# Optimization experiments

Measured on AMD Instinct MI355X. Metric: run time of the kernel, lower is better.

Reference implementation:

```python
import jax, jax.numpy as jnp
import numpy as np

H, B, D, C = 6, 512, 2048, 1000   # heads (5 ICs + backbone exit), batch, feat dim, classes
TAU = 0.5                          # confidence_threshold


def setup_inputs() -> dict:
    key = jax.random.key(0)
    k1, k2, k3, k4 = jax.random.split(key, 4)
    feats = jax.random.normal(k1, (H, B, D), dtype=jnp.float32)          # pooled reps at each exit
    W = jax.random.normal(k2, (H, D, C), dtype=jnp.float32) * 0.07       # per-head classifier weights
    b = jax.random.normal(k3, (H, C), dtype=jnp.float32) * 0.1
    y_true = jax.random.randint(k4, (B,), 0, C)
    return {"feats": feats, "W": W, "b": b, "y_true": y_true}


def reference(feats, W, b, y_true):
    # Per-head logits for every sample (vectorized replacement for the shrinking-batch loop).
    logits = jnp.einsum('hbd,hdc->hbc', feats, W) + b[:, None, :]        # [H, B, C]
    logp = jax.nn.log_softmax(logits, axis=-1)
    conf = jnp.exp(logp).max(axis=-1)                                    # [H, B] max softmax prob (prob_conf=True)

    # Early-exit routing: first head with conf >= TAU; else head with max confidence
    # (argmax returns the first occurrence, matching the strict '>' update in find_exit).
    exited = conf >= TAU                                                  # [H, B]
    any_exit = exited.any(axis=0)                                         # [B]
    first_exit = jnp.argmax(exited, axis=0)                               # [B] first True along heads
    best_conf = jnp.argmax(conf, axis=0)                                  # [B] fallback exit
    exit_idx = jnp.where(any_exit, first_exit, best_conf)                 # [B] == sample_exited_at

    # Gather the chosen head's logits per sample (vectorized masked-scatter of sample_outputs).
    outputs = jnp.take_along_axis(logits, exit_idx[None, :, None], axis=0)[0]   # [B, C]

    # criterion_ic: cross-entropy loss + accuracy on routed outputs
    out_logp = jax.nn.log_softmax(outputs, axis=-1)
    loss = -jnp.take_along_axis(out_logp, y_true[:, None], axis=1).mean()
    acc = (outputs.argmax(axis=-1) == y_true).astype(jnp.float32).mean()
    return outputs, exit_idx.astype(jnp.int32), loss, acc
```

## Files before the change

kernel.cpp:

```cpp
#include <hip/hip_runtime.h>
#include <hip/hip_bf16.h>
#include <math.h>

#define Hn 6
#define Bn 512
#define Dn 2048
#define Cn 1000
#define Cpad 1024
#define TAUv 0.5f
#define KSPLIT 2
#define KPER (Dn / KSPLIT)
#define NIT (KPER / 32)

typedef unsigned int u32;
typedef unsigned short u16;
typedef __attribute__((ext_vector_type(8))) short short8;
typedef __attribute__((ext_vector_type(4))) float f32x4;

union FragU { u32 d[4]; short8 s; };

__device__ __forceinline__ u32 cvt_pk2(float f0, float f1) {
  union { __hip_bfloat162 h; u32 u; } cv;
  cv.h = __float22bfloat162_rn(make_float2(f0, f1));
  return cv.u;
}

__device__ __forceinline__ void pack8f(const float* f, FragU& hi, FragU& lo) {
  float r[8];
#pragma unroll
  for (int i = 0; i < 4; ++i) {
    const u32 d = cvt_pk2(f[2 * i], f[2 * i + 1]);
    hi.d[i] = d;
    r[2 * i]     = f[2 * i]     - __uint_as_float(d << 16);
    r[2 * i + 1] = f[2 * i + 1] - __uint_as_float(d & 0xffff0000u);
  }
#pragma unroll
  for (int i = 0; i < 4; ++i) lo.d[i] = cvt_pk2(r[2 * i], r[2 * i + 1]);
}

__device__ __forceinline__ void dma16(const void* g, void* l) {
  __builtin_amdgcn_global_load_lds(
      (const __attribute__((address_space(1))) u32*)g,
      (__attribute__((address_space(3))) u32*)l, 16, 0, 0);
}

__global__ __launch_bounds__(256, 3) void gemm_k(
    const float* __restrict__ feats, const float* __restrict__ W,
    const float* __restrict__ bias, float* __restrict__ logits)
{
  const int h  = blockIdx.z >> 1;
  const int kz = blockIdx.z & 1;
  const int m0 = blockIdx.y * 128;
  const int n0 = blockIdx.x * 64;
  const int t = threadIdx.x, lane = t & 63, w = t >> 6;

  __shared__ __align__(16) float lds[2][6144];

  const int rA = (w & 1) * 64 + (lane >> 3);
  const int qA = (lane & 7) ^ ((lane >> 3) & 7);
  const float* gsrcA = feats + ((size_t)(h * Bn + m0 + rA)) * Dn + kz * KPER + qA * 4;
  const size_t gciA = (size_t)8 * Dn;
  const int dstA = w * 8192 + lane * 16;

  const int kb = (w - 2) * 16 + (lane >> 4);
  const int cB = lane & 15;
  const float* Wrow = W + ((size_t)h * Dn + kz * KPER) * Cn;
  const int dstB = 16384 + (w - 2) * 4096 + lane * 16;

  const int fl = lane & 15, fq = lane >> 4;
  const int wm = (w & 1) * 64, wn = (w >> 1) * 32;
  const int sxor = fl & 7;

  f32x4 acc[4][2];
#pragma unroll
  for (int i = 0; i < 4; ++i)
#pragma unroll
    for (int j = 0; j < 2; ++j) acc[i][j] = (f32x4){0.f, 0.f, 0.f, 0.f};

#define STAGE(TILE)                                                                   \
  {                                                                                   \
    char* sb = (char*)&lds[(TILE) & 1][0];                                            \
    if (w < 2) {                                                                      \
      const float* g = gsrcA + (size_t)(TILE) * 32;                                   \
      _Pragma("unroll")                                                               \
      for (int i = 0; i < 8; ++i) dma16(g + i * gciA, sb + dstA + i * 1024);          \
    } else {                                                                          \
      const size_t kt0 = (size_t)(TILE) * 32;                                         \
      _Pragma("unroll")                                                               \
      for (int i = 0; i < 4; ++i) {                                                   \
        const int kl = kb + 4 * i;                                                    \
        const int pc = cB ^ (((kl >> 3) & 1) << 2);                                   \
        int col = n0 + pc * 4;                                                        \
        col = (col + 3 < Cn) ? col : (Cn - 4);                                        \
        dma16(Wrow + (kt0 + kl) * Cn + col, sb + dstB + i * 1024);                    \
      }                                                                               \
    }                                                                                 \
  }

#define WAITCUR()                                                                     \
  {                                                                                   \
    if (w < 2) asm volatile("s_waitcnt vmcnt(8)" ::: "memory");                       \
    else       asm volatile("s_waitcnt vmcnt(4)" ::: "memory");                       \
  }

#define COMPUTE_TILE(IT)                                                              \
  {                                                                                   \
    const char*  ab = (const char*)&lds[(IT) & 1][0];                                 \
    const float* bb = (const float*)(ab + 16384);                                     \
    FragU ah[4], al[4];                                                               \
    _Pragma("unroll")                                                                 \
    for (int mt = 0; mt < 4; ++mt) {                                                  \
      const int r = wm + mt * 16 + fl;                                                \
      const float4 v0 = *(const float4*)(ab + r * 128 + ((((fq * 2)    ) ^ sxor) * 16)); \
      const float4 v1 = *(const float4*)(ab + r * 128 + ((((fq * 2) + 1) ^ sxor) * 16)); \
      float f[8] = {v0.x, v0.y, v0.z, v0.w, v1.x, v1.y, v1.z, v1.w};                  \
      pack8f(f, ah[mt], al[mt]);                                                      \
    }                                                                                 \
    _Pragma("unroll")                                                                 \
    for (int nt = 0; nt < 2; ++nt) {                                                  \
      const int n = wn + nt * 16 + fl;                                                \
      const int nsw = ((((n >> 2) ^ ((fq & 1) << 2)) << 2) | (n & 3));                \
      float f[8];                                                                     \
      _Pragma("unroll")                                                               \
      for (int e = 0; e < 8; ++e) f[e] = bb[(fq * 8 + e) * 64 + nsw];                 \
      FragU bh, bl;                                                                   \
      pack8f(f, bh, bl);                                                              \
      _Pragma("unroll")                                                               \
      for (int mt = 0; mt < 4; ++mt) {                                                \
        acc[mt][nt] = __builtin_amdgcn_mfma_f32_16x16x32_bf16(ah[mt].s, bh.s, acc[mt][nt], 0, 0, 0); \
        acc[mt][nt] = __builtin_amdgcn_mfma_f32_16x16x32_bf16(ah[mt].s, bl.s, acc[mt][nt], 0, 0, 0); \
        acc[mt][nt] = __builtin_amdgcn_mfma_f32_16x16x32_bf16(al[mt].s, bh.s, acc[mt][nt], 0, 0, 0); \
      }                                                                               \
    }                                                                                 \
  }

  STAGE(0);

  for (int it = 0; it < NIT - 1; ++it) {
    STAGE(it + 1);
    WAITCUR();
    __builtin_amdgcn_s_barrier();
    __builtin_amdgcn_sched_barrier(0);
    __builtin_amdgcn_s_setprio(1);
    COMPUTE_TILE(it);
    __builtin_amdgcn_s_setprio(0);
    __builtin_amdgcn_sched_barrier(0);
    asm volatile("s_waitcnt lgkmcnt(0)" ::: "memory");
    __builtin_amdgcn_s_barrier();
  }
  asm volatile("s_waitcnt vmcnt(0)" ::: "memory");
  __builtin_amdgcn_s_barrier();
  __builtin_amdgcn_sched_barrier(0);
  __builtin_amdgcn_s_setprio(1);
  COMPUTE_TILE(NIT - 1);
  __builtin_amdgcn_s_setprio(0);
#undef COMPUTE_TILE
#undef WAITCUR
#undef STAGE

  float* part = logits + (size_t)kz * ((size_t)Hn * Bn * Cn);
#pragma unroll
  for (int nt = 0; nt < 2; ++nt) {
    const int col = n0 + wn + nt * 16 + fl;
    if (col >= Cn) continue;
    const float bv = (kz == 0) ? bias[(size_t)h * Cn + col] : 0.f;
#pragma unroll
    for (int mt = 0; mt < 4; ++mt) {
      const int rbase = m0 + wm + mt * 16 + fq * 4;
#pragma unroll
      for (int r = 0; r < 4; ++r)
        part[((size_t)h * Bn + rbase + r) * Cn + col] = acc[mt][nt][r] + bv;
    }
  }
}

__global__ __launch_bounds__(64) void stats_k(
    const float* __restrict__ logits, float* __restrict__ msA,
    float* __restrict__ ssA, u32* __restrict__ ticket)
{
  const int id = blockIdx.x;
  const int lane = threadIdx.x;
  if (id == 0 && lane == 0) *ticket = 0;
  const size_t S = (size_t)Hn * Bn * Cn;
  const float* p = logits + (size_t)id * Cn;

  float vv[16];
#pragma unroll
  for (int i = 0; i < 4; ++i) {
    const int c4 = i * 256 + lane * 4;
    if (c4 + 3 < Cn) {
      const float4 v0 = *(const float4*)(p + c4);
      const float4 v1 = *(const float4*)(p + S + c4);
      vv[4 * i + 0] = v0.x + v1.x;
      vv[4 * i + 1] = v0.y + v1.y;
      vv[4 * i + 2] = v0.z + v1.z;
      vv[4 * i + 3] = v0.w + v1.w;
    } else {
#pragma unroll
      for (int j = 0; j < 4; ++j) {
        const int c = c4 + j;
        vv[4 * i + j] = (c < Cn) ? p[c] + p[S + c] : -3.4e38f;
      }
    }
  }
  float m = -3.4e38f;
#pragma unroll
  for (int i = 0; i < 16; ++i) m = fmaxf(m, vv[i]);
#pragma unroll
  for (int off = 32; off >= 1; off >>= 1) m = fmaxf(m, __shfl_xor(m, off));
  float s = 0.f;
#pragma unroll
  for (int i = 0; i < 16; ++i) s += (vv[i] > -3.0e38f) ? expf(vv[i] - m) : 0.f;
#pragma unroll
  for (int off = 32; off >= 1; off >>= 1) s += __shfl_xor(s, off);
  if (lane == 0) { msA[id] = m; ssA[id] = s; }
}

__global__ __launch_bounds__(256) void pick_k(
    const float* __restrict__ logits, const float* __restrict__ msA,
    const float* __restrict__ ssA, const int* __restrict__ y,
    float* __restrict__ out, float* __restrict__ out_exit,
    float* __restrict__ loss_b, float* __restrict__ corr_b,
    u32* __restrict__ ticket, float* __restrict__ scalars)
{
  const int b = blockIdx.x, tid = threadIdx.x;
  const int lane = tid & 63, w = tid >> 6;
  const size_t S = (size_t)Hn * Bn * Cn;

  int first = -1, best = 0;
  float bestc = -3.4e38f;
#pragma unroll
  for (int h = 0; h < Hn; ++h) {
    const float c = 1.0f / ssA[h * Bn + b];
    if (first < 0 && c >= TAUv) first = h;
    if (c > bestc) { bestc = c; best = h; }
  }
  const int ex = (first >= 0) ? first : best;
  const float* p = logits + ((size_t)ex * Bn + b) * Cn;

  const int c4 = tid * 4;
  float vv[4] = {-3.4e38f, -3.4e38f, -3.4e38f, -3.4e38f};
  if (c4 + 3 < Cn) {
    const float4 v0 = *(const float4*)(p + c4);
    const float4 v1 = *(const float4*)(p + S + c4);
    vv[0] = v0.x + v1.x;
    vv[1] = v0.y + v1.y;
    vv[2] = v0.z + v1.z;
    vv[3] = v0.w + v1.w;
  }
  float vm = -3.4e38f; int im = 1 << 30;
#pragma unroll
  for (int j = 0; j < 4; ++j) {
    const int c = c4 + j;
    if (c < Cn) {
      out[(size_t)b * Cn + c] = vv[j];
      if (vv[j] > vm) { vm = vv[j]; im = c; }
    }
  }
#pragma unroll
  for (int off = 32; off >= 1; off >>= 1) {
    const float ov = __shfl_xor(vm, off);
    const int   oi = __shfl_xor(im, off);
    if (ov > vm || (ov == vm && oi < im)) { vm = ov; im = oi; }
  }
  __shared__ float rm[4]; __shared__ int ri[4];
  __shared__ u32 tk;
  if (lane == 0) { rm[w] = vm; ri[w] = im; }
  __syncthreads();
  if (tid == 0) {
    float bm = rm[0]; int bi = ri[0];
    for (int q = 1; q < 4; ++q)
      if (rm[q] > bm || (rm[q] == bm && ri[q] < bi)) { bm = rm[q]; bi = ri[q]; }
    const int yt = y[b];
    const float ryt = p[yt] + p[S + yt];
    const float lp = ryt - msA[ex * Bn + b] - logf(ssA[ex * Bn + b]);
    out_exit[b] = (float)ex;
    loss_b[b] = -lp;
    corr_b[b] = (bi == yt) ? 1.f : 0.f;
    __threadfence();
    tk = atomicAdd(ticket, 1u);
  }
  __syncthreads();

  if (tk == (u32)(Bn - 1)) {
    __threadfence();
    float l = loss_b[tid] + loss_b[tid + 256];
    float c = corr_b[tid] + corr_b[tid + 256];
#pragma unroll
    for (int off = 32; off >= 1; off >>= 1) {
      l += __shfl_xor(l, off);
      c += __shfl_xor(c, off);
    }
    __shared__ float sl[4], sc[4];
    if (lane == 0) { sl[w] = l; sc[w] = c; }
    __syncthreads();
    if (tid == 0) {
      scalars[0] = (sl[0] + sl[1] + sl[2] + sl[3]) * (1.0f / (float)Bn);
      scalars[1] = (sc[0] + sc[1] + sc[2] + sc[3]) * (1.0f / (float)Bn);
    }
  }
}

extern "C" void kernel_launch(void* const* d_in, const int* in_sizes, int n_in,
                              void* d_out, int out_size, void* d_ws, size_t ws_size,
                              hipStream_t stream) {
  const float* feats = (const float*)d_in[0];
  const float* W     = (const float*)d_in[1];
  const float* bias  = (const float*)d_in[2];
  const int*   y     = (const int*)d_in[3];
  float* out = (float*)d_out;

  float* logits = (float*)d_ws;
  float* loss_b = logits + (size_t)KSPLIT * Hn * Bn * Cn;
  float* corr_b = loss_b + Bn;
  float* msA    = corr_b + Bn;
  float* ssA    = msA + Hn * Bn;
  u32*   ticket = (u32*)(ssA + Hn * Bn);
  float* out_exit    = out + (size_t)Bn * Cn;
  float* out_scalars = out + (size_t)Bn * Cn + Bn;

  gemm_k<<<dim3(Cpad / 64, Bn / 128, Hn * KSPLIT), 256, 0, stream>>>(
      feats, W, bias, logits);
  stats_k<<<Hn * Bn, 64, 0, stream>>>(logits, msA, ssA, ticket);
  pick_k<<<Bn, 256, 0, stream>>>(logits, msA, ssA, y, out, out_exit,
                                 loss_b, corr_b, ticket, out_scalars);
}
```

Before: 186.7 us.

## Fuse GEMM, softmax stats, and exit routing into one persistent kernel with grid barriers

Merges the three separate kernels into a single launch of 768 blocks that synchronize through atomic-counter grid barriers between the GEMM, row-statistics, and routing/loss stages. The stats stage maps one wave per (head, sample) row and the pick stage uses the first 512 blocks. This removes the inter-kernel launch gaps and tail drains, but adds a memset of the counters and spin-wait barriers. It relies on all blocks being co-resident, otherwise it would deadlock.

```diff
diff --git a/kernel.cpp b/kernel.cpp
--- a/kernel.cpp
+++ b/kernel.cpp
@@ -11,6 +11,7 @@
 #define KSPLIT 2
 #define KPER (Dn / KSPLIT)
 #define NIT (KPER / 32)
+#define NBLK 768
 
 typedef unsigned int u32;
 typedef unsigned short u16;
@@ -44,14 +45,31 @@
       (__attribute__((address_space(3))) u32*)l, 16, 0, 0);
 }
 
-__global__ __launch_bounds__(256, 3) void gemm_k(
+__device__ __forceinline__ void grid_barrier(u32* cnt, int tid) {
+  __syncthreads();
+  if (tid == 0) {
+    __threadfence();
+    atomicAdd(cnt, 1u);
+    while (__hip_atomic_load(cnt, __ATOMIC_RELAXED, __HIP_MEMORY_SCOPE_AGENT) < (u32)NBLK)
+      __builtin_amdgcn_s_sleep(8);
+  }
+  __syncthreads();
+  __threadfence();
+}
+
+__global__ __launch_bounds__(256, 3) void fused_k(
     const float* __restrict__ feats, const float* __restrict__ W,
-    const float* __restrict__ bias, float* __restrict__ logits)
+    const float* __restrict__ bias, float* logits,
+    const int* __restrict__ y, float* __restrict__ out,
+    float* __restrict__ out_exit, float* __restrict__ loss_b,
+    float* __restrict__ corr_b, float* __restrict__ msA,
+    float* __restrict__ ssA, u32* cnts, float* __restrict__ scalars)
 {
   const int h  = blockIdx.z >> 1;
   const int kz = blockIdx.z & 1;
   const int m0 = blockIdx.y * 128;
   const int n0 = blockIdx.x * 64;
+  const int bid = blockIdx.x + 16 * (blockIdx.y + 4 * blockIdx.z);
   const int t = threadIdx.x, lane = t & 63, w = t >> 6;
 
   __shared__ __align__(16) float lds[2][6144];
@@ -172,131 +190,120 @@
         part[((size_t)h * Bn + rbase + r) * Cn + col] = acc[mt][nt][r] + bv;
     }
   }
-}
-
-__global__ __launch_bounds__(64) void stats_k(
-    const float* __restrict__ logits, float* __restrict__ msA,
-    float* __restrict__ ssA, u32* __restrict__ ticket)
-{
-  const int id = blockIdx.x;
-  const int lane = threadIdx.x;
-  if (id == 0 && lane == 0) *ticket = 0;
+
+  grid_barrier(&cnts[0], t);
+
   const size_t S = (size_t)Hn * Bn * Cn;
-  const float* p = logits + (size_t)id * Cn;
-
-  float vv[16];
-#pragma unroll
-  for (int i = 0; i < 4; ++i) {
-    const int c4 = i * 256 + lane * 4;
+  {
+    const int id = bid * 4 + w;
+    const float* p = logits + (size_t)id * Cn;
+    float vv[16];
+#pragma unroll
+    for (int i = 0; i < 4; ++i) {
+      const int c4 = i * 256 + lane * 4;
+      if (c4 + 3 < Cn) {
+        const float4 v0 = *(const float4*)(p + c4);
+        const float4 v1 = *(const float4*)(p + S + c4);
+        vv[4 * i + 0] = v0.x + v1.x;
+        vv[4 * i + 1] = v0.y + v1.y;
+        vv[4 * i + 2] = v0.z + v1.z;
+        vv[4 * i + 3] = v0.w + v1.w;
+      } else {
+#pragma unroll
+        for (int j = 0; j < 4; ++j) {
+          const int c = c4 + j;
+          vv[4 * i + j] = (c < Cn) ? p[c] + p[S + c] : -3.4e38f;
+        }
+      }
+    }
+    float m = -3.4e38f;
+#pragma unroll
+    for (int i = 0; i < 16; ++i) m = fmaxf(m, vv[i]);
+#pragma unroll
+    for (int off = 32; off >= 1; off >>= 1) m = fmaxf(m, __shfl_xor(m, off));
+    float s = 0.f;
+#pragma unroll
+    for (int i = 0; i < 16; ++i) s += (vv[i] > -3.0e38f) ? expf(vv[i] - m) : 0.f;
+#pragma unroll
+    for (int off = 32; off >= 1; off >>= 1) s += __shfl_xor(s, off);
+    if (lane == 0) { msA[id] = m; ssA[id] = s; }
+  }
+
+  grid_barrier(&cnts[1], t);
+
+  if (bid < Bn) {
+    const int b = bid;
+    int first = -1, best = 0;
+    float bestc = -3.4e38f;
+#pragma unroll
+    for (int hh = 0; hh < Hn; ++hh) {
+      const float c = 1.0f / ssA[hh * Bn + b];
+      if (first < 0 && c >= TAUv) first = hh;
+      if (c > bestc) { bestc = c; best = hh; }
+    }
+    const int ex = (first >= 0) ? first : best;
+    const float* p = logits + ((size_t)ex * Bn + b) * Cn;
+
+    const int c4 = t * 4;
+    float vv[4] = {-3.4e38f, -3.4e38f, -3.4e38f, -3.4e38f};
     if (c4 + 3 < Cn) {
       const float4 v0 = *(const float4*)(p + c4);
       const float4 v1 = *(const float4*)(p + S + c4);
-      vv[4 * i + 0] = v0.x + v1.x;
-      vv[4 * i + 1] = v0.y + v1.y;
-      vv[4 * i + 2] = v0.z + v1.z;
-      vv[4 * i + 3] = v0.w + v1.w;
-    } else {
-#pragma unroll
-      for (int j = 0; j < 4; ++j) {
-        const int c = c4 + j;
-        vv[4 * i + j] = (c < Cn) ? p[c] + p[S + c] : -3.4e38f;
+      vv[0] = v0.x + v1.x;
+      vv[1] = v0.y + v1.y;
+      vv[2] = v0.z + v1.z;
+      vv[3] = v0.w + v1.w;
+    }
+    float vm = -3.4e38f; int im = 1 << 30;
+#pragma unroll
+    for (int j = 0; j < 4; ++j) {
+      const int c = c4 + j;
+      if (c < Cn) {
+        out[(size_t)b * Cn + c] = vv[j];
+        if (vv[j] > vm) { vm = vv[j]; im = c; }
       }
     }
-  }
-  float m = -3.4e38f;
-#pragma unroll
-  for (int i = 0; i < 16; ++i) m = fmaxf(m, vv[i]);
-#pragma unroll
-  for (int off = 32; off >= 1; off >>= 1) m = fmaxf(m, __shfl_xor(m, off));
-  float s = 0.f;
-#pragma unroll
-  for (int i = 0; i < 16; ++i) s += (vv[i] > -3.0e38f) ? expf(vv[i] - m) : 0.f;
-#pragma unroll
-  for (int off = 32; off >= 1; off >>= 1) s += __shfl_xor(s, off);
-  if (lane == 0) { msA[id] = m; ssA[id] = s; }
-}
-
-__global__ __launch_bounds__(256) void pick_k(
-    const float* __restrict__ logits, const float* __restrict__ msA,
-    const float* __restrict__ ssA, const int* __restrict__ y,
-    float* __restrict__ out, float* __restrict__ out_exit,
-    float* __restrict__ loss_b, float* __restrict__ corr_b,
-    u32* __restrict__ ticket, float* __restrict__ scalars)
-{
-  const int b = blockIdx.x, tid = threadIdx.x;
-  const int lane = tid & 63, w = tid >> 6;
-  const size_t S = (size_t)Hn * Bn * Cn;
-
-  int first = -1, best = 0;
-  float bestc = -3.4e38f;
-#pragma unroll
-  for (int h = 0; h < Hn; ++h) {
-    const float c = 1.0f / ssA[h * Bn + b];
-    if (first < 0 && c >= TAUv) first = h;
-    if (c > bestc) { bestc = c; best = h; }
-  }
-  const int ex = (first >= 0) ? first : best;
-  const float* p = logits + ((size_t)ex * Bn + b) * Cn;
-
-  const int c4 = tid * 4;
-  float vv[4] = {-3.4e38f, -3.4e38f, -3.4e38f, -3.4e38f};
-  if (c4 + 3 < Cn) {
-    const float4 v0 = *(const float4*)(p + c4);
-    const float4 v1 = *(const float4*)(p + S + c4);
-    vv[0] = v0.x + v1.x;
-    vv[1] = v0.y + v1.y;
-    vv[2] = v0.z + v1.z;
-    vv[3] = v0.w + v1.w;
-  }
-  float vm = -3.4e38f; int im = 1 << 30;
-#pragma unroll
-  for (int j = 0; j < 4; ++j) {
-    const int c = c4 + j;
-    if (c < Cn) {
-      out[(size_t)b * Cn + c] = vv[j];
-      if (vv[j] > vm) { vm = vv[j]; im = c; }
-    }
-  }
-#pragma unroll
-  for (int off = 32; off >= 1; off >>= 1) {
-    const float ov = __shfl_xor(vm, off);
-    const int   oi = __shfl_xor(im, off);
-    if (ov > vm || (ov == vm && oi < im)) { vm = ov; im = oi; }
-  }
-  __shared__ float rm[4]; __shared__ int ri[4];
-  __shared__ u32 tk;
-  if (lane == 0) { rm[w] = vm; ri[w] = im; }
-  __syncthreads();
-  if (tid == 0) {
-    float bm = rm[0]; int bi = ri[0];
-    for (int q = 1; q < 4; ++q)
-      if (rm[q] > bm || (rm[q] == bm && ri[q] < bi)) { bm = rm[q]; bi = ri[q]; }
-    const int yt = y[b];
-    const float ryt = p[yt] + p[S + yt];
-    const float lp = ryt - msA[ex * Bn + b] - logf(ssA[ex * Bn + b]);
-    out_exit[b] = (float)ex;
-    loss_b[b] = -lp;
-    corr_b[b] = (bi == yt) ? 1.f : 0.f;
-    __threadfence();
-    tk = atomicAdd(ticket, 1u);
-  }
-  __syncthreads();
-
-  if (tk == (u32)(Bn - 1)) {
-    __threadfence();
-    float l = loss_b[tid] + loss_b[tid + 256];
-    float c = corr_b[tid] + corr_b[tid + 256];
 #pragma unroll
     for (int off = 32; off >= 1; off >>= 1) {
-      l += __shfl_xor(l, off);
-      c += __shfl_xor(c, off);
-    }
-    __shared__ float sl[4], sc[4];
-    if (lane == 0) { sl[w] = l; sc[w] = c; }
+      const float ov = __shfl_xor(vm, off);
+      const int   oi = __shfl_xor(im, off);
+      if (ov > vm || (ov == vm && oi < im)) { vm = ov; im = oi; }
+    }
+    __shared__ float rm[4]; __shared__ int ri[4];
+    __shared__ u32 tk;
+    if (lane == 0) { rm[w] = vm; ri[w] = im; }
     __syncthreads();
-    if (tid == 0) {
-      scalars[0] = (sl[0] + sl[1] + sl[2] + sl[3]) * (1.0f / (float)Bn);
-      scalars[1] = (sc[0] + sc[1] + sc[2] + sc[3]) * (1.0f / (float)Bn);
+    if (t == 0) {
+      float bm = rm[0]; int bi = ri[0];
+      for (int q = 1; q < 4; ++q)
+        if (rm[q] > bm || (rm[q] == bm && ri[q] < bi)) { bm = rm[q]; bi = ri[q]; }
+      const int yt = y[b];
+      const float ryt = p[yt] + p[S + yt];
+      const float lp = ryt - msA[ex * Bn + b] - logf(ssA[ex * Bn + b]);
+      out_exit[b] = (float)ex;
+      loss_b[b] = -lp;
+      corr_b[b] = (bi == yt) ? 1.f : 0.f;
+      __threadfence();
+      tk = atomicAdd(&cnts[2], 1u);
+    }
+    __syncthreads();
+
+    if (tk == (u32)(Bn - 1)) {
+      __threadfence();
+      float l = loss_b[t] + loss_b[t + 256];
+      float c = corr_b[t] + corr_b[t + 256];
+#pragma unroll
+      for (int off = 32; off >= 1; off >>= 1) {
+        l += __shfl_xor(l, off);
+        c += __shfl_xor(c, off);
+      }
+      __shared__ float sl[4], sc[4];
+      if (lane == 0) { sl[w] = l; sc[w] = c; }
+      __syncthreads();
+      if (t == 0) {
+        scalars[0] = (sl[0] + sl[1] + sl[2] + sl[3]) * (1.0f / (float)Bn);
+        scalars[1] = (sc[0] + sc[1] + sc[2] + sc[3]) * (1.0f / (float)Bn);
+      }
     }
   }
 }
@@ -315,13 +322,12 @@
   float* corr_b = loss_b + Bn;
   float* msA    = corr_b + Bn;
   float* ssA    = msA + Hn * Bn;
-  u32*   ticket = (u32*)(ssA + Hn * Bn);
+  u32*   cnts   = (u32*)(ssA + Hn * Bn);
   float* out_exit    = out + (size_t)Bn * Cn;
   float* out_scalars = out + (size_t)Bn * Cn + Bn;
 
-  gemm_k<<<dim3(Cpad / 64, Bn / 128, Hn * KSPLIT), 256, 0, stream>>>(
-      feats, W, bias, logits);
-  stats_k<<<Hn * Bn, 64, 0, stream>>>(logits, msA, ssA, ticket);
-  pick_k<<<Bn, 256, 0, stream>>>(logits, msA, ssA, y, out, out_exit,
-                                 loss_b, corr_b, ticket, out_scalars);
-}
+  hipMemsetAsync(cnts, 0, 3 * sizeof(u32), stream);
+  fused_k<<<dim3(Cpad / 64, Bn / 128, Hn * KSPLIT), 256, 0, stream>>>(
+      feats, W, bias, logits, y, out, out_exit, loss_b, corr_b,
+      msA, ssA, cnts, out_scalars);
+}
```

Measured after the change: 451.8 us. 142% more time.

## Pre-split W into bf16 hi/lo fragment layout in a separate conversion kernel

Applied to the files above, without the earlier changes.

Adds a kernel that converts W once per call into bf16 hi/lo pairs stored in an MFMA-fragment-friendly padded layout. The GEMM then DMAs those pre-packed fragments and loads them directly as short8, instead of reading fp32 W and splitting it per tile in every block that shares it. The GEMM grid is also flattened and its block indices remapped, probably for better L2 locality. The cost is an extra launch plus a full write and reread of W in the packed form, which uses the same number of bytes as the fp32 original.

```diff
diff --git a/kernel.cpp b/kernel.cpp
--- a/kernel.cpp
+++ b/kernel.cpp
@@ -11,6 +11,7 @@
 #define KSPLIT 2
 #define KPER (Dn / KSPLIT)
 #define NIT (KPER / 32)
+#define NKT (Dn / 32)
 
 typedef unsigned int u32;
 typedef unsigned short u16;
@@ -38,20 +39,73 @@
   for (int i = 0; i < 4; ++i) lo.d[i] = cvt_pk2(r[2 * i], r[2 * i + 1]);
 }
 
+__device__ __forceinline__ void pack8v(const float* rr, uint4& hv, uint4& lv) {
+  FragU h, l;
+  pack8f(rr, h, l);
+  hv = make_uint4(h.d[0], h.d[1], h.d[2], h.d[3]);
+  lv = make_uint4(l.d[0], l.d[1], l.d[2], l.d[3]);
+}
+
 __device__ __forceinline__ void dma16(const void* g, void* l) {
   __builtin_amdgcn_global_load_lds(
       (const __attribute__((address_space(1))) u32*)g,
       (__attribute__((address_space(3))) u32*)l, 16, 0, 0);
 }
 
+__global__ __launch_bounds__(256) void convW_k(
+    const float* __restrict__ W, u16* __restrict__ Bh, u16* __restrict__ Bl)
+{
+  __shared__ float smem[32 * 129];
+  const int t  = blockIdx.x;
+  const int n0 = blockIdx.y * 128;
+  const int h  = blockIdx.z;
+  const int tid = threadIdx.x;
+
+#pragma unroll
+  for (int i = 0; i < 4; ++i) {
+    const int f = i * 256 + tid;
+    const int k = f >> 5, q = f & 31;
+    const int n = n0 + q * 4;
+    const float* src = W + ((size_t)h * Dn + t * 32 + k) * Cn;
+    float4 v = make_float4(0.f, 0.f, 0.f, 0.f);
+    if (n + 3 < Cn) {
+      v = *(const float4*)(src + n);
+    } else {
+      if (n + 0 < Cn) v.x = src[n + 0];
+      if (n + 1 < Cn) v.y = src[n + 1];
+      if (n + 2 < Cn) v.z = src[n + 2];
+      if (n + 3 < Cn) v.w = src[n + 3];
+    }
+    smem[k * 129 + q * 4 + 0] = v.x; smem[k * 129 + q * 4 + 1] = v.y;
+    smem[k * 129 + q * 4 + 2] = v.z; smem[k * 129 + q * 4 + 3] = v.w;
+  }
+  __syncthreads();
+#pragma unroll
+  for (int i = 0; i < 2; ++i) {
+    const int j = i * 256 + tid;
+    const int c = j >> 7, n = j & 127;
+    float rr[8];
+#pragma unroll
+    for (int e = 0; e < 8; ++e) rr[e] = smem[(c * 8 + e) * 129 + n];
+    uint4 hv, lv;
+    pack8v(rr, hv, lv);
+    const size_t o = (((size_t)(h * NKT + t) * 4 + c) * Cpad + n0 + n);
+    ((uint4*)Bh)[o] = hv;
+    ((uint4*)Bl)[o] = lv;
+  }
+}
+
 __global__ __launch_bounds__(256, 3) void gemm_k(
-    const float* __restrict__ feats, const float* __restrict__ W,
-    const float* __restrict__ bias, float* __restrict__ logits)
+    const float* __restrict__ feats, const u16* __restrict__ BhG,
+    const u16* __restrict__ BlG, const float* __restrict__ bias,
+    float* __restrict__ logits)
 {
-  const int h  = blockIdx.z >> 1;
-  const int kz = blockIdx.z & 1;
-  const int m0 = blockIdx.y * 128;
-  const int n0 = blockIdx.x * 64;
+  const int wg = (blockIdx.x & 7) * 96 + (blockIdx.x >> 3);
+  const int n0 = (wg & 15) * 64;
+  const int m0 = ((wg >> 4) & 3) * 128;
+  const int z  = wg >> 6;
+  const int h  = z >> 1;
+  const int kz = z & 1;
   const int t = threadIdx.x, lane = t & 63, w = t >> 6;
 
   __shared__ __align__(16) float lds[2][6144];
@@ -62,9 +116,8 @@
   const size_t gciA = (size_t)8 * Dn;
   const int dstA = w * 8192 + lane * 16;
 
-  const int kb = (w - 2) * 16 + (lane >> 4);
-  const int cB = lane & 15;
-  const float* Wrow = W + ((size_t)h * Dn + kz * KPER) * Cn;
+  const uint4* bsrcG = (const uint4*)((w == 2) ? BhG : BlG)
+                     + ((size_t)h * NKT) * 4 * Cpad + n0 + lane;
   const int dstB = 16384 + (w - 2) * 4096 + lane * 16;
 
   const int fl = lane & 15, fq = lane >> 4;
@@ -85,15 +138,10 @@
       _Pragma("unroll")                                                               \
       for (int i = 0; i < 8; ++i) dma16(g + i * gciA, sb + dstA + i * 1024);          \
     } else {                                                                          \
-      const size_t kt0 = (size_t)(TILE) * 32;                                         \
+      const int kt = kz * NIT + (TILE);                                               \
+      const uint4* g = bsrcG + (size_t)(kt * 4) * Cpad;                               \
       _Pragma("unroll")                                                               \
-      for (int i = 0; i < 4; ++i) {                                                   \
-        const int kl = kb + 4 * i;                                                    \
-        const int pc = cB ^ (((kl >> 3) & 1) << 2);                                   \
-        int col = n0 + pc * 4;                                                        \
-        col = (col + 3 < Cn) ? col : (Cn - 4);                                        \
-        dma16(Wrow + (kt0 + kl) * Cn + col, sb + dstB + i * 1024);                    \
-      }                                                                               \
+      for (int i = 0; i < 4; ++i) dma16(g + (size_t)i * Cpad, sb + dstB + i * 1024);  \
     }                                                                                 \
   }
 
@@ -105,8 +153,9 @@
 
 #define COMPUTE_TILE(IT)                                                              \
   {                                                                                   \
-    const char*  ab = (const char*)&lds[(IT) & 1][0];                                 \
-    const float* bb = (const float*)(ab + 16384);                                     \
+    const char* ab  = (const char*)&lds[(IT) & 1][0];                                 \
+    const u16*  bbh = (const u16*)(ab + 16384);                                       \
+    const u16*  bbl = (const u16*)(ab + 16384 + 4096);                                \
     FragU ah[4], al[4];                                                               \
     _Pragma("unroll")                                                                 \
     for (int mt = 0; mt < 4; ++mt) {                                                  \
@@ -119,12 +168,9 @@
     _Pragma("unroll")                                                                 \
     for (int nt = 0; nt < 2; ++nt) {                                                  \
       const int n = wn + nt * 16 + fl;                                                \
-      const int nsw = ((((n >> 2) ^ ((fq & 1) << 2)) << 2) | (n & 3));                \
-      float f[8];                                                                     \
-      _Pragma("unroll")                                                               \
-      for (int e = 0; e < 8; ++e) f[e] = bb[(fq * 8 + e) * 64 + nsw];                 \
       FragU bh, bl;                                                                   \
-      pack8f(f, bh, bl);                                                              \
+      bh.s = *(const short8*)(bbh + (size_t)(fq * 64 + n) * 8);                       \
+      bl.s = *(const short8*)(bbl + (size_t)(fq * 64 + n) * 8);                       \
       _Pragma("unroll")                                                               \
       for (int mt = 0; mt < 4; ++mt) {                                                \
         acc[mt][nt] = __builtin_amdgcn_mfma_f32_16x16x32_bf16(ah[mt].s, bh.s, acc[mt][nt], 0, 0, 0); \
@@ -316,11 +362,13 @@
   float* msA    = corr_b + Bn;
   float* ssA    = msA + Hn * Bn;
   u32*   ticket = (u32*)(ssA + Hn * Bn);
+  u16*   BhG    = (u16*)(ticket + 64);
+  u16*   BlG    = BhG + (size_t)Hn * NKT * 4 * Cpad * 8;
   float* out_exit    = out + (size_t)Bn * Cn;
   float* out_scalars = out + (size_t)Bn * Cn + Bn;
 
-  gemm_k<<<dim3(Cpad / 64, Bn / 128, Hn * KSPLIT), 256, 0, stream>>>(
-      feats, W, bias, logits);
+  convW_k<<<dim3(NKT, 8, Hn), 256, 0, stream>>>(W, BhG, BlG);
+  gemm_k<<<dim3(768, 1, 1), 256, 0, stream>>>(feats, BhG, BlG, bias, logits);
   stats_k<<<Hn * Bn, 64, 0, stream>>>(logits, msA, ssA, ticket);
   pick_k<<<Bn, 256, 0, stream>>>(logits, msA, ssA, y, out, out_exit,
                                  loss_b, corr_b, ticket, out_scalars);
```

Result: slower. 193.6 us (+3.7%).
